# Kernel optimization log

Measured on AMD Instinct MI355X. Metric: run time of the kernel, lower is better.

The kernel has to match this reference:

```python
import jax, jax.numpy as jnp
import numpy as np

D_MODEL = 1024
N_HEADS = 16
SEQ = 2048
BATCH = 2
EPS = 1e-5


def layer_norm(x, g, b):
    mu = jnp.mean(x, axis=-1, keepdims=True)
    var = jnp.mean(jnp.square(x - mu), axis=-1, keepdims=True)
    return (x - mu) * jax.lax.rsqrt(var + EPS) * g + b


def setup_inputs() -> dict:
    key = jax.random.key(0)
    ks = jax.random.split(key, 10)
    D = D_MODEL
    s = lambda fan_in: 1.0 / np.sqrt(fan_in)
    return {
        "x": jax.random.normal(ks[0], (BATCH, SEQ, D), dtype=jnp.float32),
        # weights stored [in, out] (torch Linear is y = x @ W.T; equivalent math)
        "w_attn": jax.random.uniform(ks[1], (D, 3 * D), minval=-s(D), maxval=s(D), dtype=jnp.float32),
        "b_attn": jnp.zeros((3 * D,), jnp.float32),
        "w_proj": jax.random.uniform(ks[2], (D, D), minval=-s(D), maxval=s(D), dtype=jnp.float32),
        "b_proj": jnp.zeros((D,), jnp.float32),
        "ln1_g": jnp.ones((D,), jnp.float32),
        "ln1_b": jnp.zeros((D,), jnp.float32),
        "ln2_g": jnp.ones((D,), jnp.float32),
        "ln2_b": jnp.zeros((D,), jnp.float32),
        "w_fc1": jax.random.uniform(ks[3], (D, 4 * D), minval=-s(D), maxval=s(D), dtype=jnp.float32),
        "b_fc1": jnp.zeros((4 * D,), jnp.float32),
        "w_fc2": jax.random.uniform(ks[4], (4 * D, D), minval=-s(4 * D), maxval=s(4 * D), dtype=jnp.float32),
        "b_fc2": jnp.zeros((D,), jnp.float32),
    }


def reference(x, w_attn, b_attn, w_proj, b_proj, ln1_g, ln1_b, ln2_g, ln2_b, w_fc1, b_fc1, w_fc2, b_fc2):
    B, L, D = x.shape
    H = N_HEADS
    Dh = D // H

    # --- attention sublayer ---
    h = layer_norm(x, ln1_g, ln1_b)
    qkv = h @ w_attn + b_attn                      # [B, L, 3D]
    # SOURCE BUG (faithful): q, k, v are all taken from the k third.
    k = qkv[..., D:2 * D]
    kh = k.reshape(B, L, H, Dh).transpose(0, 2, 1, 3)   # [B, H, L, Dh]
    att = jnp.einsum('bhqd,bhkd->bhqk', kh, kh) / jnp.sqrt(jnp.float32(Dh))
    att = jax.nn.softmax(att, axis=-1)
    out = jnp.einsum('bhqk,bhkd->bhqd', att, kh)         # [B, H, L, Dh]
    out = out.transpose(0, 2, 1, 3).reshape(B, L, D)
    x = x + (out @ w_proj + b_proj)

    # --- feed-forward sublayer ---
    h = layer_norm(x, ln2_g, ln2_b)
    h = jax.nn.relu(h @ w_fc1 + b_fc1)
    x = x + (h @ w_fc2 + b_fc2)
    return x
```

## Files before the change

### kernel.cpp

```cpp
#include <hip/hip_runtime.h>


typedef __attribute__((ext_vector_type(8))) short s8v;
typedef __attribute__((ext_vector_type(4))) short s4v;
typedef __attribute__((ext_vector_type(4))) float f4v;

#define D_MODEL 1024
#define SEQ 2048
#define BATCH 2
#define NH 16
#define DH 64
#define MROWS (BATCH * SEQ)

#define KH_SCALE 0.42466088f
#define KH_ISCALE 2.3548200f

__device__ __forceinline__ float b2f(unsigned short u) {
  union { unsigned int i; float f; } v; v.i = ((unsigned int)u) << 16; return v.f;
}
__device__ __forceinline__ unsigned short f2b(float f) {
  unsigned int i = __builtin_bit_cast(unsigned int, f);
  unsigned int r = (i + 0x7fffu + ((i >> 16) & 1u)) >> 16;
  return (unsigned short)r;
}
__device__ __forceinline__ void async16(const void* g, void* l) {
  __builtin_amdgcn_global_load_lds(
      (const __attribute__((address_space(1))) unsigned int*)g,
      (__attribute__((address_space(3))) unsigned int*)l, 16, 0, 0);
}
__device__ __forceinline__ unsigned short cvt_b(float f) { return f2b(f); }
__device__ __forceinline__ unsigned short cvt_b(unsigned short u) { return u; }

__device__ __forceinline__ float xp2(float x) {
#if __has_builtin(__builtin_amdgcn_exp2f)
  return __builtin_amdgcn_exp2f(x);
#else
  return exp2f(x);
#endif
}

__device__ __forceinline__ s4v cvt4(float a, float b, float c, float d) {
  unsigned int lo, hi;
  asm("v_cvt_pk_bf16_f32 %0, %1, %2" : "=v"(lo) : "v"(a), "v"(b));
  asm("v_cvt_pk_bf16_f32 %0, %1, %2" : "=v"(hi) : "v"(c), "v"(d));
  union { unsigned long long u; s4v v; } u;
  u.u = ((unsigned long long)hi << 32) | (unsigned long long)lo;
  return u.v;
}

#if __has_builtin(__builtin_amdgcn_mfma_f32_16x16x16_bf16)
__device__ __forceinline__ f4v mfma16(s4v a, s4v b, f4v c) {
  return __builtin_amdgcn_mfma_f32_16x16x16_bf16(a, b, c, 0, 0, 0);
}
#elif __has_builtin(__builtin_amdgcn_mfma_f32_16x16x16bf16_1k)
__device__ __forceinline__ f4v mfma16(s4v a, s4v b, f4v c) {
  return __builtin_amdgcn_mfma_f32_16x16x16bf16_1k(a, b, c, 0, 0, 0);
}
#else
__device__ __forceinline__ f4v mfma16(s4v a, s4v b, f4v c) {
  s8v aa = {a[0], a[1], a[2], a[3], 0, 0, 0, 0};
  s8v bb = {b[0], b[1], b[2], b[3], 0, 0, 0, 0};
  return __builtin_amdgcn_mfma_f32_16x16x32_bf16(aa, bb, c, 0, 0, 0);
}
#endif

__device__ __forceinline__ int xcd_swz(int bidl, int nwg) {
  return (nwg & 7) ? bidl : ((bidl & 7) * (nwg >> 3) + (bidl >> 3));
}

__global__ __launch_bounds__(256) void ln_kernel(
    const float* __restrict__ x, const float* __restrict__ g,
    const float* __restrict__ bb, unsigned short* __restrict__ out) {
  int row = blockIdx.x;
  int t = threadIdx.x;
  const float* xr = x + (size_t)row * D_MODEL;
  float v[4];
  float s = 0.f, s2 = 0.f;
#pragma unroll
  for (int i = 0; i < 4; ++i) {
    float f = xr[t + 256 * i];
    v[i] = f; s += f; s2 += f * f;
  }
#pragma unroll
  for (int off = 1; off < 64; off <<= 1) {
    s += __shfl_xor(s, off, 64);
    s2 += __shfl_xor(s2, off, 64);
  }
  __shared__ float red[8];
  if ((t & 63) == 0) { red[t >> 6] = s; red[4 + (t >> 6)] = s2; }
  __syncthreads();
  s = red[0] + red[1] + red[2] + red[3];
  s2 = red[4] + red[5] + red[6] + red[7];
  float mu = s * (1.f / D_MODEL);
  float var = s2 * (1.f / D_MODEL) - mu * mu;
  float rstd = rsqrtf(var + 1e-5f);
#pragma unroll
  for (int i = 0; i < 4; ++i) {
    int c = t + 256 * i;
    float h = (v[i] - mu) * rstd * g[c] + bb[c];
    out[(size_t)row * D_MODEL + c] = f2b(h);
  }
}

template <typename T>
__global__ __launch_bounds__(256) void transpose_b(
    const T* __restrict__ src, unsigned short* __restrict__ dst,
    int srcStride, int dstStride, long long srcBatch, long long dstBatch) {
  __shared__ unsigned short tile[64][65];
  const T* s = src + (size_t)blockIdx.z * srcBatch;
  unsigned short* d = dst + (size_t)blockIdx.z * dstBatch;
  int n0 = blockIdx.x * 64, k0 = blockIdx.y * 64;
  for (int i = threadIdx.x; i < 4096; i += 256) {
    int k = i >> 6, n = i & 63;
    tile[k][n] = cvt_b(s[(size_t)(k0 + k) * srcStride + n0 + n]);
  }
  __syncthreads();
  for (int i = threadIdx.x; i < 4096; i += 256) {
    int n = i >> 6, k = i & 63;
    d[(size_t)(n0 + n) * dstStride + k0 + k] = tile[k][n];
  }
}

template <int RES, bool RELU, bool KH, int OUTF, int BM, int BN>
__global__ __launch_bounds__(256) void gemm_bt(
    const unsigned short* __restrict__ A, const unsigned short* __restrict__ Bt,
    const float* __restrict__ bias, const float* __restrict__ res,
    void* __restrict__ out, int M, int N, int K) {
  constexpr int MT = BM / 32;
  constexpr int NT = BN / 32;
  __shared__ __align__(16) unsigned short lsA[2][BM * 64];
  __shared__ __align__(16) unsigned short lsB[2][BN * 64];
  int tid = threadIdx.x;
  int lane = tid & 63, w = tid >> 6, quad = lane >> 4, l16 = lane & 15;
  int bidl = blockIdx.y * (int)gridDim.x + blockIdx.x;
  int swz = xcd_swz(bidl, (int)(gridDim.x * gridDim.y));
  int m0 = (swz / (int)gridDim.x) * BM, n0 = (swz % (int)gridDim.x) * BN;
  int wm = (w >> 1) * (BM / 2), wn = (w & 1) * (BN / 2);
  f4v acc[MT][NT] = {};

  auto stage = [&](int bsel, int ktE) {
#pragma unroll
    for (int i = 0; i < MT; ++i) {
      int cb = w * (BM * 2) + i * 64;
      int ci = cb + lane;
      int row = ci >> 3, c = ci & 7;
      int cs = c ^ (row & 7);
      async16(A + (size_t)(m0 + row) * K + ktE + cs * 8, &lsA[bsel][cb * 8]);
    }
#pragma unroll
    for (int i = 0; i < NT; ++i) {
      int cb = w * (BN * 2) + i * 64;
      int ci = cb + lane;
      int row = ci >> 3, c = ci & 7;
      int cs = c ^ (row & 7);
      async16(Bt + (size_t)(n0 + row) * K + ktE + cs * 8, &lsB[bsel][cb * 8]);
    }
  };

  stage(0, 0);
  int nK = K >> 6;
  for (int kt = 0; kt < nK; ++kt) {
    int b = kt & 1;
    if (kt + 1 < nK) {
      stage(b ^ 1, (kt + 1) << 6);
      if constexpr (MT + NT == 4)      asm volatile("s_waitcnt vmcnt(4)" ::: "memory");
      else if constexpr (MT + NT == 6) asm volatile("s_waitcnt vmcnt(6)" ::: "memory");
      else                             asm volatile("s_waitcnt vmcnt(8)" ::: "memory");
    } else {
      asm volatile("s_waitcnt vmcnt(0)" ::: "memory");
    }
    __builtin_amdgcn_sched_barrier(0);
    __builtin_amdgcn_s_barrier();
    __builtin_amdgcn_sched_barrier(0);
#pragma unroll
    for (int s = 0; s < 2; ++s) {
      s8v af[MT], bf[NT];
#pragma unroll
      for (int t = 0; t < MT; ++t) {
        int am = wm + t * 16 + l16;
        int ac = (s * 4 + quad) ^ (am & 7);
        af[t] = *(const s8v*)(&lsA[b][am * 64 + ac * 8]);
      }
#pragma unroll
      for (int t = 0; t < NT; ++t) {
        int bn = wn + t * 16 + l16;
        int bc = (s * 4 + quad) ^ (bn & 7);
        bf[t] = *(const s8v*)(&lsB[b][bn * 64 + bc * 8]);
      }
#pragma unroll
      for (int ti = 0; ti < MT; ++ti)
#pragma unroll
        for (int tj = 0; tj < NT; ++tj)
          acc[ti][tj] = __builtin_amdgcn_mfma_f32_16x16x32_bf16(
              af[ti], bf[tj], acc[ti][tj], 0, 0, 0);
    }
    asm volatile("s_waitcnt lgkmcnt(0)" ::: "memory");
    __builtin_amdgcn_sched_barrier(0);
    __builtin_amdgcn_s_barrier();
    __builtin_amdgcn_sched_barrier(0);
  }
#pragma unroll
  for (int tj = 0; tj < NT; ++tj) {
    int col = n0 + wn + tj * 16 + l16;
    float bv = bias[col];
#pragma unroll
    for (int ti = 0; ti < MT; ++ti) {
#pragma unroll
      for (int r = 0; r < 4; ++r) {
        int rowg = m0 + wm + ti * 16 + quad * 4 + r;
        float vv = acc[ti][tj][r] + bv;
        if (KH) vv *= KH_SCALE;
        if (RES == 2) vv += res[(size_t)rowg * N + col];
        if (RELU) vv = fmaxf(vv, 0.f);
        size_t oidx;
        if (KH) {
          int b2 = rowg >> 11, l = rowg & 2047, h = col >> 6, d = col & 63;
          oidx = (((size_t)(b2 * NH + h)) * SEQ + l) * DH + d;
        } else {
          oidx = (size_t)rowg * N + col;
        }
        if (OUTF == 0) ((unsigned short*)out)[oidx] = f2b(vv);
        else           ((float*)out)[oidx] = vv;
      }
    }
  }
}

__global__ __launch_bounds__(256) void gemm_proj(
    const unsigned short* __restrict__ Opart, const float* __restrict__ lpart,
    const unsigned short* __restrict__ Bt, const float* __restrict__ bias,
    const float* __restrict__ res, float* __restrict__ out, int M, int N, int K) {
  __shared__ __align__(16) unsigned short lsA[2][64 * 64];
  __shared__ __align__(16) unsigned short lsB[2][64 * 64];
  int tid = threadIdx.x;
  int lane = tid & 63, w = tid >> 6, quad = lane >> 4, l16 = lane & 15;
  int bidl = blockIdx.y * (int)gridDim.x + blockIdx.x;
  int swz = xcd_swz(bidl, (int)(gridDim.x * gridDim.y));
  int m0 = (swz / (int)gridDim.x) * 64, n0 = (swz % (int)gridDim.x) * 64;
  int wm = (w >> 1) * 32, wn = (w & 1) * 32;
  f4v acc[2][2] = {};

  int ci_[2], csA[2], mA[2], b2A[2], lA[2];
#pragma unroll
  for (int i = 0; i < 2; ++i) {
    int cb = w * 128 + i * 64;
    int ci = cb + lane;
    int row = ci >> 3, c = ci & 7;
    ci_[i] = ci; csA[i] = c ^ (row & 7);
    mA[i] = m0 + row; b2A[i] = mA[i] >> 11; lA[i] = mA[i] & 2047;
  }
  s8v o0r[2], o1r[2];
  float lsr0[2], lsr1[2];
  auto issueA = [&](int kt) {
#pragma unroll
    for (int i = 0; i < 2; ++i) {
      const unsigned short* pa =
          Opart + (size_t)mA[i] * D_MODEL + kt * 64 + csA[i] * 8;
      o0r[i] = *(const s8v*)pa;
      o1r[i] = *(const s8v*)(pa + (size_t)MROWS * D_MODEL);
      size_t lidx = ((size_t)b2A[i] * NH + kt) * SEQ + lA[i];
      lsr0[i] = lpart[lidx];
      lsr1[i] = lpart[(size_t)BATCH * NH * SEQ + lidx];
    }
  };
  auto issueB = [&](int bsel, int ktE) {
#pragma unroll
    for (int i = 0; i < 2; ++i) {
      int cb = w * 128 + i * 64;
      int ci = cb + lane;
      int row = ci >> 3, c = ci & 7;
      int cs = c ^ (row & 7);
      async16(Bt + (size_t)(n0 + row) * K + ktE + cs * 8, &lsB[bsel][cb * 8]);
    }
  };
  auto combineWrite = [&](int bsel) {
#pragma unroll
    for (int i = 0; i < 2; ++i) {
      float inv = KH_ISCALE / (lsr0[i] + lsr1[i]);
      float f[8];
#pragma unroll
      for (int j = 0; j < 8; ++j)
        f[j] = (b2f((unsigned short)o0r[i][j]) +
                b2f((unsigned short)o1r[i][j])) * inv;
      s4v lo = cvt4(f[0], f[1], f[2], f[3]);
      s4v hi = cvt4(f[4], f[5], f[6], f[7]);
      s8v vv = {lo[0], lo[1], lo[2], lo[3], hi[0], hi[1], hi[2], hi[3]};
      *(s8v*)(&lsA[bsel][ci_[i] * 8]) = vv;
    }
  };

  issueA(0); issueB(0, 0);
  __builtin_amdgcn_sched_barrier(0);
  asm volatile("s_waitcnt vmcnt(2)" ::: "memory");
  __builtin_amdgcn_sched_barrier(0);
  combineWrite(0);
  asm volatile("s_waitcnt lgkmcnt(0)" ::: "memory");
  __builtin_amdgcn_sched_barrier(0);

  int nK = K >> 6;
  for (int kt = 0; kt < nK; ++kt) {
    int b = kt & 1;
    if (kt + 1 < nK) {
      issueA(kt + 1); issueB(b ^ 1, (kt + 1) << 6);
      __builtin_amdgcn_sched_barrier(0);
      asm volatile("s_waitcnt vmcnt(10)" ::: "memory");
    } else {
      __builtin_amdgcn_sched_barrier(0);
      asm volatile("s_waitcnt vmcnt(0)" ::: "memory");
    }
    __builtin_amdgcn_sched_barrier(0);
    __builtin_amdgcn_s_barrier();
    __builtin_amdgcn_sched_barrier(0);
#pragma unroll
    for (int s = 0; s < 2; ++s) {
      s8v af[2], bf[2];
#pragma unroll
      for (int t = 0; t < 2; ++t) {
        int am = wm + t * 16 + l16;
        int ac = (s * 4 + quad) ^ (am & 7);
        af[t] = *(const s8v*)(&lsA[b][am * 64 + ac * 8]);
      }
#pragma unroll
      for (int t = 0; t < 2; ++t) {
        int bn = wn + t * 16 + l16;
        int bc = (s * 4 + quad) ^ (bn & 7);
        bf[t] = *(const s8v*)(&lsB[b][bn * 64 + bc * 8]);
      }
#pragma unroll
      for (int ti = 0; ti < 2; ++ti)
#pragma unroll
        for (int tj = 0; tj < 2; ++tj)
          acc[ti][tj] = __builtin_amdgcn_mfma_f32_16x16x32_bf16(
              af[ti], bf[tj], acc[ti][tj], 0, 0, 0);
    }
    if (kt + 1 < nK) {
      __builtin_amdgcn_sched_barrier(0);
      asm volatile("s_waitcnt vmcnt(2)" ::: "memory");
      __builtin_amdgcn_sched_barrier(0);
      combineWrite(b ^ 1);
    }
    asm volatile("s_waitcnt lgkmcnt(0)" ::: "memory");
    __builtin_amdgcn_sched_barrier(0);
    __builtin_amdgcn_s_barrier();
    __builtin_amdgcn_sched_barrier(0);
  }
#pragma unroll
  for (int tj = 0; tj < 2; ++tj) {
    int col = n0 + wn + tj * 16 + l16;
    float bv = bias[col];
#pragma unroll
    for (int ti = 0; ti < 2; ++ti) {
#pragma unroll
      for (int r = 0; r < 4; ++r) {
        int rowg = m0 + wm + ti * 16 + quad * 4 + r;
        float vv = acc[ti][tj][r] + bv + res[(size_t)rowg * N + col];
        out[(size_t)rowg * N + col] = vv;
      }
    }
  }
}

__global__ __launch_bounds__(256) void flash_k(
    const unsigned short* __restrict__ kh, const unsigned short* __restrict__ khT,
    unsigned short* __restrict__ Opart, float* __restrict__ lpart) {
  __shared__ __align__(16) unsigned short lsK[128 * 64];
  __shared__ __align__(16) unsigned short lsKT[64 * 128];
  int tid = threadIdx.x;
  int lane = tid & 63, w = tid >> 6, quad = lane >> 4, l16 = lane & 15;
  int split = blockIdx.x, bh = blockIdx.y, qb = blockIdx.z;
  const unsigned short* khB = kh + (size_t)bh * SEQ * DH;
  const unsigned short* khTB = khT + (size_t)bh * DH * SEQ;
  unsigned short* Op = Opart + (size_t)split * MROWS * D_MODEL;
  float* lp = lpart + (size_t)split * BATCH * NH * SEQ;
  s8v aQ[2][2];
#pragma unroll
  for (int g = 0; g < 2; ++g) {
    int q = qb * 128 + w * 32 + g * 16 + l16;
#pragma unroll
    for (int s = 0; s < 2; ++s)
      aQ[g][s] = *(const s8v*)(khB + (size_t)q * DH + s * 32 + quad * 8);
  }
  const s4v vone = {(short)0x3F80, (short)0x3F80, (short)0x3F80, (short)0x3F80};
  f4v accO[2][4] = {};
  f4v accL[2] = {};

  for (int kt8 = 0; kt8 < 8; ++kt8) {
    int key0 = split * 1024 + kt8 * 128;
#pragma unroll
    for (int i = 0; i < 4; ++i) {
      int cb = w * 256 + i * 64;
      int ci = cb + lane;
      int row = ci >> 3, c = ci & 7;
      int cs = c ^ (row & 7);
      async16(khB + (size_t)(key0 + row) * DH + cs * 8, &lsK[cb * 8]);
    }
#pragma unroll
    for (int i = 0; i < 4; ++i) {
      int cb = w * 256 + i * 64;
      int ci = cb + lane;
      int row = ci >> 4, c = ci & 15;
      int cs = c ^ (row & 15);
      async16(khTB + (size_t)row * SEQ + key0 + cs * 8, &lsKT[cb * 8]);
    }
    __builtin_amdgcn_s_waitcnt(0x0f70);
    __syncthreads();
#pragma unroll
    for (int half = 0; half < 2; ++half) {
      f4v accST[2][4] = {};
#pragma unroll
      for (int s = 0; s < 2; ++s) {
#pragma unroll
        for (int tj = 0; tj < 4; ++tj) {
          int key = half * 64 + tj * 16 + l16;
          int c = (s * 4 + quad) ^ (key & 7);
          s8v kf = *(const s8v*)(&lsK[key * 64 + c * 8]);
#pragma unroll
          for (int g = 0; g < 2; ++g)
            accST[g][tj] = __builtin_amdgcn_mfma_f32_16x16x32_bf16(
                kf, aQ[g][s], accST[g][tj], 0, 0, 0);
        }
      }
#pragma unroll
      for (int tj = 0; tj < 4; ++tj) {
        s4v pf[2];
#pragma unroll
        for (int g = 0; g < 2; ++g) {
          float p0 = xp2(accST[g][tj][0]);
          float p1 = xp2(accST[g][tj][1]);
          float p2 = xp2(accST[g][tj][2]);
          float p3 = xp2(accST[g][tj][3]);
          pf[g] = cvt4(p0, p1, p2, p3);
          accL[g] = mfma16(pf[g], vone, accL[g]);
        }
#pragma unroll
        for (int db = 0; db < 4; ++db) {
          int d = db * 16 + l16;
          int ch = (half * 8 + tj * 2 + (quad >> 1)) ^ (d & 15);
          s4v vf = *(const s4v*)(&lsKT[d * 128 + ch * 8 + (quad & 1) * 4]);
#pragma unroll
          for (int g = 0; g < 2; ++g)
            accO[g][db] = mfma16(pf[g], vf, accO[g][db]);
        }
      }
    }
    __syncthreads();
  }
  int b = bh >> 4, h = bh & 15;
#pragma unroll
  for (int g = 0; g < 2; ++g) {
    if (l16 == 0) {
#pragma unroll
      for (int r = 0; r < 4; ++r) {
        int q = qb * 128 + w * 32 + g * 16 + quad * 4 + r;
        lp[(size_t)bh * SEQ + q] = accL[g][r];
      }
    }
#pragma unroll
    for (int r = 0; r < 4; ++r) {
      int l = qb * 128 + w * 32 + g * 16 + quad * 4 + r;
#pragma unroll
      for (int db = 0; db < 4; ++db) {
        int d = db * 16 + l16;
        Op[((size_t)(b * SEQ + l)) * D_MODEL + h * DH + d] = f2b(accO[g][db][r]);
      }
    }
  }
}

extern "C" void kernel_launch(void* const* d_in, const int* in_sizes, int n_in,
                              void* d_out, int out_size, void* d_ws, size_t ws_size,
                              hipStream_t stream) {
  (void)in_sizes; (void)n_in; (void)out_size;
  const float* x      = (const float*)d_in[0];
  const float* w_attn = (const float*)d_in[1];
  const float* b_attn = (const float*)d_in[2];
  const float* w_proj = (const float*)d_in[3];
  const float* b_proj = (const float*)d_in[4];
  const float* ln1_g  = (const float*)d_in[5];
  const float* ln1_b  = (const float*)d_in[6];
  const float* ln2_g  = (const float*)d_in[7];
  const float* ln2_b  = (const float*)d_in[8];
  const float* w_fc1  = (const float*)d_in[9];
  const float* b_fc1  = (const float*)d_in[10];
  const float* w_fc2  = (const float*)d_in[11];
  const float* b_fc2  = (const float*)d_in[12];

  char* ws = (char*)d_ws;
  unsigned short* Opart = (unsigned short*)ws;
  unsigned short* kh    = (unsigned short*)(ws + (size_t)(16u << 20));
  unsigned short* khT   = (unsigned short*)(ws + (size_t)(24u << 20));
  float*          x1    = (float*)(ws + (size_t)(32u << 20));
  unsigned short* hbuf  = (unsigned short*)(ws + (size_t)(48u << 20));
  float*          lpart = (float*)(ws + (size_t)(48u << 20));
  float* outf = (float*)d_out;
  bool big_ws = ws_size >= ((size_t)72u << 20);

  unsigned short* wTk;
  unsigned short* wTp;
  unsigned short* wTf1;
  unsigned short* wTf2;
  unsigned short* fc1o;
  if (big_ws) {
    wTk  = (unsigned short*)(ws + (size_t)(56u << 20));
    wTp  = wTk;
    wTf1 = wTk;
    wTf2 = (unsigned short*)(ws + (size_t)(64u << 20));
    fc1o = (unsigned short*)ws;
  } else {
    wTk  = (unsigned short*)ws;
    wTp  = kh;
    wTf1 = (unsigned short*)ws;
    wTf2 = (unsigned short*)(ws + (size_t)(8u << 20));
    fc1o = kh;
  }

  dim3 blk(256);
  hipLaunchKernelGGL(ln_kernel, dim3(MROWS), blk, 0, stream, x, ln1_g, ln1_b, hbuf);
  hipLaunchKernelGGL(transpose_b<float>, dim3(16, 16, 1), blk, 0, stream,
                     w_attn + 1024, wTk, 3 * D_MODEL, D_MODEL, 0LL, 0LL);
  hipLaunchKernelGGL((gemm_bt<0, false, true, 0, 64, 64>), dim3(16, 64), blk, 0,
                     stream, hbuf, wTk, b_attn + 1024, nullptr, (void*)kh,
                     MROWS, D_MODEL, D_MODEL);
  hipLaunchKernelGGL(transpose_b<unsigned short>, dim3(1, 32, 32), blk, 0, stream,
                     kh, khT, DH, SEQ, (long long)(SEQ * DH), (long long)(DH * SEQ));
  hipLaunchKernelGGL(flash_k, dim3(2, 32, SEQ / 128), blk, 0, stream,
                     kh, khT, Opart, lpart);
  hipLaunchKernelGGL(transpose_b<float>, dim3(16, 16, 1), blk, 0, stream,
                     w_proj, wTp, D_MODEL, D_MODEL, 0LL, 0LL);
  hipLaunchKernelGGL(gemm_proj, dim3(16, 64), blk, 0, stream,
                     Opart, lpart, wTp, b_proj, x, x1,
                     MROWS, D_MODEL, D_MODEL);
  hipLaunchKernelGGL(ln_kernel, dim3(MROWS), blk, 0, stream, x1, ln2_g, ln2_b, hbuf);
  hipLaunchKernelGGL(transpose_b<float>, dim3(64, 16, 1), blk, 0, stream,
                     w_fc1, wTf1, 4 * D_MODEL, D_MODEL, 0LL, 0LL);
  hipLaunchKernelGGL(transpose_b<float>, dim3(16, 64, 1), blk, 0, stream,
                     w_fc2, wTf2, D_MODEL, 4 * D_MODEL, 0LL, 0LL);
  if (big_ws) {
    hipLaunchKernelGGL((gemm_bt<0, true, false, 0, 128, 64>), dim3(64, 32), blk, 0,
                       stream, hbuf, wTf1, b_fc1, nullptr, (void*)fc1o,
                       MROWS, 4 * D_MODEL, D_MODEL);
    hipLaunchKernelGGL((gemm_bt<2, false, false, 1, 64, 64>), dim3(16, 64), blk, 0,
                       stream, fc1o, wTf2, b_fc2, x1, (void*)outf,
                       MROWS, D_MODEL, 4 * D_MODEL);
  } else {
    for (int c = 0; c < 2; ++c) {
      const unsigned short* h2c = hbuf + (size_t)c * 2048 * D_MODEL;
      const float* x1c = x1 + (size_t)c * 2048 * D_MODEL;
      float* outc = outf + (size_t)c * 2048 * D_MODEL;
      hipLaunchKernelGGL((gemm_bt<0, true, false, 0, 128, 64>), dim3(64, 16), blk, 0,
                         stream, h2c, wTf1, b_fc1, nullptr, (void*)fc1o,
                         2048, 4 * D_MODEL, D_MODEL);
      hipLaunchKernelGGL((gemm_bt<2, false, false, 1, 64, 64>), dim3(16, 32), blk, 0,
                         stream, fc1o, wTf2, b_fc2, x1c, (void*)outc,
                         2048, D_MODEL, 4 * D_MODEL);
    }
  }
}
```

Baseline: 341.5 us.

## Add 256x256-tile 8-wave pipelined GEMM for the FC1 layer

Adds a new bf16 MFMA GEMM kernel with 256x256 output tiles, 512 threads and double-buffered async global-to-LDS loads interleaved with compute phases. It uses XOR-swizzled LDS, explicit barriers and s_setprio. The FC1 matmul (with bias and ReLU) now uses this kernel in the big-workspace path. The larger tiles raise data reuse and the finer-grained prefetch overlaps loads with MFMA, at the cost of high register use and lower occupancy. The grid shrinks to 256 blocks, which may underfill the GPU.

Measured after the change: 331.4 us. 3.0% less time.

```diff
diff --git a/kernel.cpp b/kernel.cpp
--- a/kernel.cpp
+++ b/kernel.cpp
@@ -221,6 +221,122 @@
         }
         if (OUTF == 0) ((unsigned short*)out)[oidx] = f2b(vv);
         else           ((float*)out)[oidx] = vv;
+      }
+    }
+  }
+}
+
+__global__ __launch_bounds__(512, 2) void gemm256(
+    const unsigned short* __restrict__ A, const unsigned short* __restrict__ Bt,
+    const float* __restrict__ bias, unsigned short* __restrict__ out,
+    bool relu, int M, int N, int K) {
+  __shared__ __align__(16) unsigned short lsA[2][2][128 * 64];
+  __shared__ __align__(16) unsigned short lsB[2][2][128 * 64];
+  int tid = threadIdx.x;
+  int lane = tid & 63, w = tid >> 6, quad = lane >> 4, l16 = lane & 15;
+  int wr = w >> 2, wc = w & 3;
+  int bidl = blockIdx.y * (int)gridDim.x + blockIdx.x;
+  int swz = xcd_swz(bidl, (int)(gridDim.x * gridDim.y));
+  int m0 = (swz / (int)gridDim.x) * 256, n0 = (swz % (int)gridDim.x) * 256;
+  f4v acc[8][4] = {};
+
+  auto stageA = [&](int par, int h, int kt) {
+#pragma unroll
+    for (int i = 0; i < 2; ++i) {
+      int cb = w * 128 + i * 64;
+      int ci = cb + lane;
+      int r = ci >> 3, c = ci & 7;
+      int cs = c ^ (r & 7);
+      int grow = ((r >> 6) << 7) + h * 64 + (r & 63);
+      async16(A + (size_t)(m0 + grow) * K + kt * 64 + cs * 8,
+              &lsA[par][h][cb * 8]);
+    }
+  };
+  auto stageB = [&](int par, int h, int kt) {
+#pragma unroll
+    for (int i = 0; i < 2; ++i) {
+      int cb = w * 128 + i * 64;
+      int ci = cb + lane;
+      int r = ci >> 3, c = ci & 7;
+      int cs = c ^ (r & 7);
+      int gn = ((r >> 5) << 6) + h * 32 + (r & 31);
+      async16(Bt + (size_t)(n0 + gn) * K + kt * 64 + cs * 8,
+              &lsB[par][h][cb * 8]);
+    }
+  };
+
+#define PHASE(PAR, MH, NH, STAGE_STMT, VMN)                                    \
+  {                                                                            \
+    s8v af[4][2], bf[2][2];                                                    \
+    _Pragma("unroll") for (int tm = 0; tm < 4; ++tm) {                         \
+      int lr = wr * 64 + tm * 16 + l16;                                        \
+      _Pragma("unroll") for (int s = 0; s < 2; ++s) {                          \
+        int ac = (s * 4 + quad) ^ (lr & 7);                                    \
+        af[tm][s] = *(const s8v*)(&lsA[PAR][MH][lr * 64 + ac * 8]);            \
+      }                                                                        \
+    }                                                                          \
+    _Pragma("unroll") for (int tn = 0; tn < 2; ++tn) {                         \
+      int rb = wc * 32 + tn * 16 + l16;                                        \
+      _Pragma("unroll") for (int s = 0; s < 2; ++s) {                          \
+        int bc = (s * 4 + quad) ^ (rb & 7);                                    \
+        bf[tn][s] = *(const s8v*)(&lsB[PAR][NH][rb * 64 + bc * 8]);            \
+      }                                                                        \
+    }                                                                          \
+    STAGE_STMT;                                                                \
+    __builtin_amdgcn_sched_barrier(0);                                         \
+    __builtin_amdgcn_s_barrier();                                              \
+    __builtin_amdgcn_sched_barrier(0);                                         \
+    __builtin_amdgcn_s_setprio(1);                                             \
+    _Pragma("unroll") for (int s = 0; s < 2; ++s)                              \
+      _Pragma("unroll") for (int tm = 0; tm < 4; ++tm)                         \
+        _Pragma("unroll") for (int tn = 0; tn < 2; ++tn)                       \
+          acc[MH * 4 + tm][NH * 2 + tn] =                                      \
+              __builtin_amdgcn_mfma_f32_16x16x32_bf16(                         \
+                  af[tm][s], bf[tn][s], acc[MH * 4 + tm][NH * 2 + tn], 0, 0, 0);\
+    __builtin_amdgcn_s_setprio(0);                                             \
+    __builtin_amdgcn_sched_barrier(0);                                         \
+    if (VMN == 4) { asm volatile("s_waitcnt vmcnt(4)" ::: "memory"); }         \
+    else if (VMN == 0) { asm volatile("s_waitcnt vmcnt(0)" ::: "memory"); }    \
+    __builtin_amdgcn_sched_barrier(0);                                         \
+    __builtin_amdgcn_s_barrier();                                              \
+    __builtin_amdgcn_sched_barrier(0);                                         \
+  }
+
+  int nT = K >> 6;
+  stageA(0, 0, 0); stageB(0, 0, 0); stageA(0, 1, 0); stageB(0, 1, 0);
+  stageB(1, 0, 1); stageA(1, 0, 1);
+  asm volatile("s_waitcnt vmcnt(4)" ::: "memory");
+  __builtin_amdgcn_sched_barrier(0);
+  __builtin_amdgcn_s_barrier();
+  __builtin_amdgcn_sched_barrier(0);
+
+  for (int t = 0; t < nT; t += 2) {
+    bool s2 = (t + 2) < nT, s3 = (t + 3) < nT;
+    PHASE(0, 0, 0, { stageA(1, 1, t + 1); }, -1)
+    PHASE(0, 1, 0, { stageB(1, 1, t + 1); }, -1)
+    PHASE(0, 0, 1, { if (s2) stageB(0, 0, t + 2); }, -1)
+    PHASE(0, 1, 1, { if (s2) stageA(0, 0, t + 2); }, (s2 ? 4 : 0))
+    PHASE(1, 0, 0, { if (s2) stageA(0, 1, t + 2); }, -1)
+    PHASE(1, 1, 0, { if (s2) stageB(0, 1, t + 2); }, -1)
+    PHASE(1, 0, 1, { if (s3) stageB(1, 0, t + 3); }, -1)
+    PHASE(1, 1, 1, { if (s3) stageA(1, 0, t + 3); }, (s3 ? 4 : 0))
+  }
+#undef PHASE
+
+#pragma unroll
+  for (int mi = 0; mi < 8; ++mi) {
+    int mh = mi >> 2, tm = mi & 3;
+#pragma unroll
+    for (int nj = 0; nj < 4; ++nj) {
+      int nh = nj >> 1, tn = nj & 1;
+      int col = n0 + wc * 64 + nh * 32 + tn * 16 + l16;
+      float bv = bias[col];
+#pragma unroll
+      for (int r = 0; r < 4; ++r) {
+        int rowg = m0 + wr * 128 + mh * 64 + tm * 16 + quad * 4 + r;
+        float vv = acc[mi][nj][r] + bv;
+        if (relu) vv = fmaxf(vv, 0.f);
+        out[(size_t)rowg * N + col] = f2b(vv);
       }
     }
   }
@@ -536,8 +652,8 @@
   hipLaunchKernelGGL(transpose_b<float>, dim3(16, 64, 1), blk, 0, stream,
                      w_fc2, wTf2, D_MODEL, 4 * D_MODEL, 0LL, 0LL);
   if (big_ws) {
-    hipLaunchKernelGGL((gemm_bt<0, true, false, 0, 128, 64>), dim3(64, 32), blk, 0,
-                       stream, hbuf, wTf1, b_fc1, nullptr, (void*)fc1o,
+    hipLaunchKernelGGL(gemm256, dim3(16, 16), dim3(512), 0, stream,
+                       hbuf, wTf1, b_fc1, fc1o, true,
                        MROWS, 4 * D_MODEL, D_MODEL);
     hipLaunchKernelGGL((gemm_bt<2, false, false, 1, 64, 64>), dim3(16, 64), blk, 0,
                        stream, fc1o, wTf2, b_fc2, x1, (void*)outf,
```
